# Kernel tuning notes

Measured on AMD Instinct MI355X. Metric: run time of the kernel, lower is better.

Reference implementation:

```python
import jax, jax.numpy as jnp
import numpy as np

B, N, L, H, D, IN = 512, 128, 10, 16, 8, 16
NT = B * N
E = NT * 16

def _lin(key, fan_in, shape):
    b = 1.0 / np.sqrt(fan_in)
    return jax.random.uniform(key, shape, jnp.float32, -b, b)

def setup_inputs() -> dict:
    key = jax.random.key(0)
    ks = jax.random.split(key, 12)
    x = jax.random.normal(ks[0], (NT, IN), jnp.float32)
    # within-graph random edges so to_dense_adj is well defined
    g = jax.random.randint(ks[1], (E,), 0, B)
    i = jax.random.randint(ks[2], (E,), 0, N)
    j = jax.random.randint(ks[3], (E,), 0, N)
    edge_index = jnp.stack([g * N + i, g * N + j]).astype(jnp.int32)
    return dict(
        x=x,
        gin_w1=_lin(ks[4], H, (2, L, H, H)),   # [ld/ud, layer, H, H]
        gin_b1=_lin(ks[5], H, (2, L, H)),
        gin_w2=_lin(ks[6], H, (2, L, H, H)),
        gin_b2=_lin(ks[7], H, (2, L, H)),
        mean_w=_lin(ks[8], H, (2, H, D)),
        mean_b=jnp.zeros((2, D), jnp.float32),
        std_w=_lin(ks[9], H, (2, H, D)),
        std_b=jnp.zeros((2, D), jnp.float32),
        edge_index=edge_index,
    )

def _encoder(x, w1, b1, w2, b2, mw, mb, sw, sb, src, dst):
    # PyG GIN stack: GINConv(MLP[Lin->ReLU->Lin]), eps=0, sum aggregation,
    # ReLU between layers (dropout = identity in eval mode).
    h = x
    for l in range(L):
        agg = jax.ops.segment_sum(h[src], dst, num_segments=NT)
        t = h + agg  # (1+eps)*x + sum_{j in N(i)} x_j with eps=0
        t = jnp.maximum(t @ w1[l] + b1[l], 0.0) @ w2[l] + b2[l]
        h = jnp.maximum(t, 0.0) if l < L - 1 else t
    mean = h @ mw + mb
    std = jax.nn.softplus(h @ sw + sb)
    return mean, std

def reference(x, gin_w1, gin_b1, gin_w2, gin_b2, mean_w, mean_b, std_w, std_b, edge_index):
    src, dst = edge_index[0], edge_index[1]
    enc = jax.vmap(_encoder, in_axes=(None, 0, 0, 0, 0, 0, 0, 0, 0, None, None))
    mean, std = enc(x, gin_w1, gin_b1, gin_w2, gin_b2,
                    mean_w, mean_b, std_w, std_b, src, dst)  # [2, NT, D]
    # reparameterized sample: eps ~ N(0,1) (prior.sample, detached)
    eps = jax.random.normal(jax.random.key(42), (2, NT, D), jnp.float32)
    z = mean + std * eps
    z_ld = z[0].reshape(B, N, D)
    z_ud = z[1].reshape(B, N, D)
    logits = jnp.einsum('bnd,bmd->bnm', z_ld, z_ud)  # per-graph inner-product decode
    dense_adj = jnp.zeros((B, N, N), jnp.float32).at[src // N, src % N, dst % N].add(1.0)
    n_pos = dense_adj.sum()
    posw = (B * N * N - n_pos) / n_pos
    # BCE-with-logits, pos_weight, reduction='sum'
    nll = jnp.sum(posw * dense_adj * jax.nn.softplus(-logits)
                  + (1.0 - dense_adj) * jax.nn.softplus(logits))
    # KL(N(mean,std) || N(0,1)), summed over both encoders
    kl = jnp.sum(-jnp.log(std) + 0.5 * (std * std + mean * mean) - 0.5)
    return nll, kl, jax.nn.sigmoid(logits), dense_adj
```

## Files before the change

kernel.cpp:

```cpp
#include <hip/hip_runtime.h>

#define B_    512
#define N_    128
#define L_    10
#define H_    16
#define D_    8
#define NT_   65536
#define E_    1048576
#define NNB_  8388608
#define CAP_  4096
#define CCAP_ 2816
#define HS_   20
#define PLANE_ (129*HS_ + 4)

__device__ __forceinline__ unsigned rotl32(unsigned v, int r){ return (v<<r)|(v>>(32-r)); }

__device__ __forceinline__ void threefry2x32(unsigned c0, unsigned c1, unsigned &o0, unsigned &o1){
  const unsigned ks0 = 0u, ks1 = 42u, ks2 = 0u ^ 42u ^ 0x1BD11BDAu;
  unsigned x0 = c0 + ks0, x1 = c1 + ks1;
#define TFR(r) { x0 += x1; x1 = rotl32(x1, r); x1 ^= x0; }
  TFR(13) TFR(15) TFR(26) TFR(6)   x0 += ks1; x1 += ks2 + 1u;
  TFR(17) TFR(29) TFR(16) TFR(24)  x0 += ks2; x1 += ks0 + 2u;
  TFR(13) TFR(15) TFR(26) TFR(6)   x0 += ks0; x1 += ks1 + 3u;
  TFR(17) TFR(29) TFR(16) TFR(24)  x0 += ks1; x1 += ks2 + 4u;
  TFR(13) TFR(15) TFR(26) TFR(6)   x0 += ks2; x1 += ks0 + 5u;
#undef TFR
  o0 = x0; o1 = x1;
}

__device__ __forceinline__ float erfinv_f(float x){
  float w = -log1pf(-x*x);
  float p;
  if (w < 5.0f) {
    w -= 2.5f;
    p = 2.81022636e-08f;
    p = fmaf(p, w, 3.43273939e-07f);
    p = fmaf(p, w, -3.5233877e-06f);
    p = fmaf(p, w, -4.39150654e-06f);
    p = fmaf(p, w, 0.00021858087f);
    p = fmaf(p, w, -0.00125372503f);
    p = fmaf(p, w, -0.00417768164f);
    p = fmaf(p, w, 0.246640727f);
    p = fmaf(p, w, 1.50140941f);
  } else {
    w = sqrtf(w) - 3.0f;
    p = -0.000200214257f;
    p = fmaf(p, w, 0.000100950558f);
    p = fmaf(p, w, 0.00134934322f);
    p = fmaf(p, w, -0.00367342844f);
    p = fmaf(p, w, 0.00573950773f);
    p = fmaf(p, w, -0.0076224613f);
    p = fmaf(p, w, 0.00943887047f);
    p = fmaf(p, w, 1.00167406f);
    p = fmaf(p, w, 2.83297682f);
  }
  return p * x;
}

__device__ __forceinline__ float softplus_f(float x){
  return fmaxf(x, 0.0f) + log1pf(expf(-fabsf(x)));
}

__device__ __forceinline__ void blockReduceAdd(double v, double* target){
  __shared__ double red[16];
  int lane = threadIdx.x & 63;
  int w    = threadIdx.x >> 6;
  #pragma unroll
  for(int off = 32; off > 0; off >>= 1) v += __shfl_down(v, off);
  if(lane == 0) red[w] = v;
  __syncthreads();
  if(threadIdx.x == 0){
    double s = red[0];
    int nw = (blockDim.x + 63) >> 6;
    for(int k = 1; k < nw; k++) s += red[k];
    atomicAdd(target, s);
  }
}

__global__ __launch_bounds__(256)
void k_bin(const int* __restrict__ ei, int* __restrict__ gcount,
           unsigned short* __restrict__ ebuf){
  __shared__ int cnt[512];
  __shared__ int gb[512];
  const int t = threadIdx.x;
  cnt[t] = 0; cnt[t + 256] = 0;
  __syncthreads();
  int kv[8];
  const int base = blockIdx.x * 2048;
  #pragma unroll
  for(int q = 0; q < 8; q++){
    int e = base + q*256 + t;
    int s = ei[e];
    int d = ei[E_ + e];
    int g = d >> 7;
    kv[q] = (g << 14) | ((s & 127) << 7) | (d & 127);
    atomicAdd(&cnt[g], 1);
  }
  __syncthreads();
  #pragma unroll
  for(int g = 0; g < 512; g += 256){
    int c = cnt[g + t];
    gb[g + t] = c ? atomicAdd(&gcount[g + t], c) : 0;
    cnt[g + t] = 0;
  }
  __syncthreads();
  #pragma unroll
  for(int q = 0; q < 8; q++){
    int g = kv[q] >> 14;
    int pos = atomicAdd(&cnt[g], 1);
    int idx = gb[g] + pos;
    if(idx < CAP_) ebuf[(size_t)g*CAP_ + idx] = (unsigned short)(kv[q] & 0x3FFF);
  }
}

__global__ __launch_bounds__(1024, 8)
void k_mega(const float* __restrict__ x, const unsigned short* __restrict__ ebuf,
            const int* __restrict__ gcount,
            const float* __restrict__ gw1, const float* __restrict__ gb1,
            const float* __restrict__ gw2, const float* __restrict__ gb2,
            const float* __restrict__ mw,  const float* __restrict__ mb,
            const float* __restrict__ sw,  const float* __restrict__ sb,
            float* __restrict__ z, double* acc){
  __shared__ __align__(16) float hh[2*PLANE_];
  __shared__ __align__(16) float agg_l[2*128*HS_];
  __shared__ __align__(16) float u_l[2*128*HS_];
  __shared__ __align__(16) unsigned short col_l[CCAP_];
  __shared__ int off_l[129];

  const int b = blockIdx.x, t = threadIdx.x;
  const int n  = t & 127;
  const int q  = __builtin_amdgcn_readfirstlane((t >> 7) & 3);
  const int e  = __builtin_amdgcn_readfirstlane(t >> 9);
  const int q4 = q * 4;

  int* cnt = (int*)hh;

  if(t < 128) cnt[t] = 0;
  {
    uint4 s128; s128.x = s128.y = s128.z = s128.w = 0x00800080u;
    uint4* c4 = (uint4*)col_l;
    if(t < CCAP_/8) c4[t] = s128;
  }
  __syncthreads();

  int ec = gcount[b]; if(ec > CAP_) ec = CAP_;
  const unsigned short* eb = ebuf + (size_t)b*CAP_;
  for(int i = t; i < ec; i += 1024) atomicAdd(&cnt[eb[i] & 127], 1);
  __syncthreads();

  if(t < 64){
    int lane = t;
    int a0 = (cnt[lane]      + 3) & ~3;
    int a1 = (cnt[64 + lane] + 3) & ~3;
    int s0 = a0, s1 = a1;
    #pragma unroll
    for(int o = 1; o < 64; o <<= 1){
      int v0 = __shfl_up(s0, o);
      int v1 = __shfl_up(s1, o);
      if(lane >= o){ s0 += v0; s1 += v1; }
    }
    int totA = __shfl(s0, 63);
    off_l[lane]      = s0 - a0;
    off_l[64 + lane] = totA + s1 - a1;
    if(lane == 63) off_l[128] = totA + s1;
    cnt[lane] = 0; cnt[64 + lane] = 0;
  }
  __syncthreads();

  for(int i = t; i < ec; i += 1024){
    int pk = eb[i];
    int d = pk & 127;
    int pos = atomicAdd(&cnt[d], 1);
    int idx = off_l[d] + pos;
    if(idx < CCAP_) col_l[idx] = (unsigned short)(pk >> 7);
  }
  __syncthreads();
  const int r0 = off_l[n], r1 = off_l[n + 1];

  if(t < 512){
    const float4* x4 = (const float4*)x + (size_t)b*512;
    float4 v = x4[t];
    int row = t >> 2, c = (t & 3)*4;
    *(float4*)&hh[row*HS_ + c]          = v;
    *(float4*)&hh[PLANE_ + row*HS_ + c] = v;
  }
  if(t < 16){ hh[128*HS_ + t] = 0.0f; hh[PLANE_ + 128*HS_ + t] = 0.0f; }
  __syncthreads();

  const float* hb   = hh    + e*PLANE_;
  float*       aggb = agg_l + e*(128*HS_);
  float*       ub   = u_l   + e*(128*HS_);
  const float* w1g = gw1 + e*(L_*256);
  const float* w2g = gw2 + e*(L_*256);
  const float* b1g = gb1 + e*(L_*16);
  const float* b2g = gb2 + e*(L_*16);

  for(int l = 0; l < L_; l++){
    float ag0, ag1, ag2, ag3;
    {
      float4 s = *(const float4*)&hb[n*HS_ + q4];
      ag0 = s.x; ag1 = s.y; ag2 = s.z; ag3 = s.w;
    }
    for(int r = r0; r < r1; r += 4){
      ushort4 c4 = *(const ushort4*)&col_l[r];
      float4 v0 = *(const float4*)&hb[c4.x*HS_ + q4];
      float4 v1 = *(const float4*)&hb[c4.y*HS_ + q4];
      float4 v2 = *(const float4*)&hb[c4.z*HS_ + q4];
      float4 v3 = *(const float4*)&hb[c4.w*HS_ + q4];
      ag0 += v0.x + v1.x + v2.x + v3.x;
      ag1 += v0.y + v1.y + v2.y + v3.y;
      ag2 += v0.z + v1.z + v2.z + v3.z;
      ag3 += v0.w + v1.w + v2.w + v3.w;
    }
    *(float4*)&aggb[n*HS_ + q4] = make_float4(ag0, ag1, ag2, ag3);
    __syncthreads();

    float av[16];
    {
      const float4* ap = (const float4*)&aggb[n*HS_];
      float4 a0 = ap[0], a1 = ap[1], a2 = ap[2], a3 = ap[3];
      av[0]=a0.x; av[1]=a0.y; av[2]=a0.z; av[3]=a0.w;
      av[4]=a1.x; av[5]=a1.y; av[6]=a1.z; av[7]=a1.w;
      av[8]=a2.x; av[9]=a2.y; av[10]=a2.z; av[11]=a2.w;
      av[12]=a3.x; av[13]=a3.y; av[14]=a3.z; av[15]=a3.w;
    }
    const float* w1c = w1g + l*256 + q4;
    float u0 = b1g[l*16 + q4 + 0];
    float u1 = b1g[l*16 + q4 + 1];
    float u2 = b1g[l*16 + q4 + 2];
    float u3 = b1g[l*16 + q4 + 3];
    #pragma unroll
    for(int k = 0; k < 16; k++){
      float a = av[k];
      const float* wr = w1c + k*16;
      u0 = fmaf(a, wr[0], u0);
      u1 = fmaf(a, wr[1], u1);
      u2 = fmaf(a, wr[2], u2);
      u3 = fmaf(a, wr[3], u3);
    }
    u0 = fmaxf(u0, 0.0f); u1 = fmaxf(u1, 0.0f);
    u2 = fmaxf(u2, 0.0f); u3 = fmaxf(u3, 0.0f);
    *(float4*)&ub[n*HS_ + q4] = make_float4(u0, u1, u2, u3);
    __syncthreads();

    float uv[16];
    {
      const float4* up = (const float4*)&ub[n*HS_];
      float4 a0 = up[0], a1 = up[1], a2 = up[2], a3 = up[3];
      uv[0]=a0.x; uv[1]=a0.y; uv[2]=a0.z; uv[3]=a0.w;
      uv[4]=a1.x; uv[5]=a1.y; uv[6]=a1.z; uv[7]=a1.w;
      uv[8]=a2.x; uv[9]=a2.y; uv[10]=a2.z; uv[11]=a2.w;
      uv[12]=a3.x; uv[13]=a3.y; uv[14]=a3.z; uv[15]=a3.w;
    }
    const float* w2c = w2g + l*256 + q4;
    float o0 = b2g[l*16 + q4 + 0];
    float o1 = b2g[l*16 + q4 + 1];
    float o2 = b2g[l*16 + q4 + 2];
    float o3 = b2g[l*16 + q4 + 3];
    #pragma unroll
    for(int k = 0; k < 16; k++){
      float a = uv[k];
      const float* wr = w2c + k*16;
      o0 = fmaf(a, wr[0], o0);
      o1 = fmaf(a, wr[1], o1);
      o2 = fmaf(a, wr[2], o2);
      o3 = fmaf(a, wr[3], o3);
    }
    if(l < L_ - 1){
      o0 = fmaxf(o0, 0.0f); o1 = fmaxf(o1, 0.0f);
      o2 = fmaxf(o2, 0.0f); o3 = fmaxf(o3, 0.0f);
    }
    *(float4*)&hh[e*PLANE_ + n*HS_ + q4] = make_float4(o0, o1, o2, o3);
    __syncthreads();
  }

  float hv[16];
  {
    const float4* hp = (const float4*)&hb[n*HS_];
    float4 a0 = hp[0], a1 = hp[1], a2 = hp[2], a3 = hp[3];
    hv[0]=a0.x; hv[1]=a0.y; hv[2]=a0.z; hv[3]=a0.w;
    hv[4]=a1.x; hv[5]=a1.y; hv[6]=a1.z; hv[7]=a1.w;
    hv[8]=a2.x; hv[9]=a2.y; hv[10]=a2.z; hv[11]=a2.w;
    hv[12]=a3.x; hv[13]=a3.y; hv[14]=a3.z; hv[15]=a3.w;
  }
  const float* mwg = mw + e*128; const float* mbg = mb + e*8;
  const float* swg = sw + e*128; const float* sbg = sb + e*8;
  double kll = 0.0;
  float zv[2];
  unsigned nodeBase = ((unsigned)e*NT_ + (unsigned)(b*128 + n))*8u;
  #pragma unroll
  for(int dd = 0; dd < 2; dd++){
    int d = q*2 + dd;
    float mm = mbg[d], ss = sbg[d];
    #pragma unroll
    for(int k = 0; k < 16; k++){
      mm = fmaf(hv[k], mwg[k*8 + d], mm);
      ss = fmaf(hv[k], swg[k*8 + d], ss);
    }
    float stdv = softplus_f(ss);
    unsigned o0, o1; threefry2x32(0u, nodeBase + (unsigned)d, o0, o1);
    unsigned bits = o0 ^ o1;
    float uu = __uint_as_float((bits >> 9) | 0x3f800000u) - 1.0f;
    const float lo = -0.99999994f;
    float uval = fmaxf(lo, fmaf(uu, 2.0f, lo));
    float eps = 1.41421356f * erfinv_f(uval);
    zv[dd] = mm + stdv * eps;
    float stdc = fmaxf(stdv, 1e-37f);
    float term = 0.5f*(stdv*stdv + mm*mm) - logf(stdc) - 0.5f;
    if(!(term == term) || term > 1e30f) term = 1e30f;
    kll += (double)term;
  }
  *(float2*)&z[nodeBase + (unsigned)(q*2)] = make_float2(zv[0], zv[1]);
  blockReduceAdd(kll, acc + 1);
}

#define TSB_ 132
__global__ __launch_bounds__(256, 8)
void k_decode(const float* __restrict__ z, const unsigned short* __restrict__ ebuf,
              const int* __restrict__ gcount, float* __restrict__ sig,
              float* __restrict__ adj, double* acc){
  __shared__ float zl[256];
  __shared__ float zu[1152];
  __shared__ unsigned tile32[32*TSB_/4];
  const int b = blockIdx.x, cy = blockIdx.y, t = threadIdx.x;
  const int row0 = cy * 32;
  const float* zld = z + (size_t)b*1024 + (size_t)row0*8;
  const float* zud = z + (size_t)NT_*8 + (size_t)b*1024;
  for(int k = t; k < 1024; k += 256) zu[(k >> 3)*9 + (k & 7)] = zud[k];
  zl[t] = zld[t];
  for(int k = t; k < 32*TSB_/4; k += 256) tile32[k] = 0u;
  __syncthreads();
  {
    int ec = gcount[b]; if(ec > CAP_) ec = CAP_;
    const unsigned short* eb = ebuf + (size_t)b*CAP_;
    for(int qq = t; qq < ec; qq += 256){
      int pk = eb[qq];
      int r = (pk >> 7) - row0;
      if((unsigned)r < 32u){
        int cell = r*TSB_ + (pk & 127);
        atomicAdd(&tile32[cell >> 2], 1u << ((cell & 3)*8));
      }
    }
  }
  __syncthreads();
  double local = 0.0;
  float* sigb = sig + (size_t)b*16384 + (size_t)row0*128;
  float* adjb = adj + (size_t)b*16384 + (size_t)row0*128;
  for(int it = 0; it < 4; it++){
    int base = it*1024 + t*4;
    int n = base >> 7, mcol = base & 127;
    const float* za = &zl[n*8];
    float xs[4];
    #pragma unroll
    for(int c = 0; c < 4; c++){
      const float* zb = &zu[(mcol + c)*9];
      float xx = 0.0f;
      #pragma unroll
      for(int d = 0; d < 8; d++) xx = fmaf(za[d], zb[d], xx);
      xs[c] = xx;
    }
    unsigned packed = tile32[(n*TSB_ + mcol) >> 2];
    float4 av;
    av.x = (float)( packed        & 0xFF);
    av.y = (float)((packed >> 8)  & 0xFF);
    av.z = (float)((packed >> 16) & 0xFF);
    av.w = (float)((packed >> 24) & 0xFF);
    float ads[4] = {av.x, av.y, av.z, av.w};
    float sgs[4];
    float fl = 0.0f;
    #pragma unroll
    for(int c = 0; c < 4; c++){
      float xx = xs[c];
      sgs[c] = 1.0f / (1.0f + expf(-xx));
      float cc  = log1pf(expf(-fabsf(xx)));
      float spp = fmaxf(xx, 0.0f) + cc;
      float spn = fmaxf(-xx, 0.0f) + cc;
      fl += 7.0f*ads[c]*spn + (1.0f - ads[c])*spp;
    }
    local += (double)fl;
    ((float4*)(sigb + base))[0] = make_float4(sgs[0], sgs[1], sgs[2], sgs[3]);
    ((float4*)(adjb + base))[0] = av;
  }
  blockReduceAdd(local, acc + 0);
}

__device__ __forceinline__ float clamp_finite(double v){
  if(v != v) return 0.0f;
  if(v >  3.3e38) return  3.3e38f;
  if(v < -3.3e38) return -3.3e38f;
  return (float)v;
}
__global__ void k_final(const double* __restrict__ acc, float* __restrict__ out){
  if(threadIdx.x == 0){
    out[0] = clamp_finite(acc[0]);
    out[1] = clamp_finite(acc[1]);
  }
}

extern "C" void kernel_launch(void* const* d_in, const int* in_sizes, int n_in,
                              void* d_out, int out_size, void* d_ws, size_t ws_size,
                              hipStream_t stream){
  const float* x   = (const float*)d_in[0];
  const float* gw1 = (const float*)d_in[1];
  const float* gb1 = (const float*)d_in[2];
  const float* gw2 = (const float*)d_in[3];
  const float* gb2 = (const float*)d_in[4];
  const float* mw  = (const float*)d_in[5];
  const float* mb  = (const float*)d_in[6];
  const float* sw  = (const float*)d_in[7];
  const float* sb  = (const float*)d_in[8];
  const int*   ei  = (const int*)d_in[9];

  float* out = (float*)d_out;
  float* sig = out + 2;
  float* adj = out + 2 + NNB_;

  char* ws = (char*)d_ws;
  int*            gcount = (int*)(ws);
  double*         acc    = (double*)(ws + 2048);
  unsigned short* ebuf   = (unsigned short*)(ws + 4096);
  float*          z      = (float*)(ws + 4096 + 2*512*CAP_);

  hipMemsetAsync(ws, 0, 4096, stream);

  k_bin   <<<E_/2048, 256, 0, stream>>>(ei, gcount, ebuf);
  k_mega  <<<B_, 1024, 0, stream>>>(x, ebuf, gcount, gw1, gb1, gw2, gb2,
                                    mw, mb, sw, sb, z, acc);
  k_decode<<<dim3(B_, 4), 256, 0, stream>>>(z, ebuf, gcount, sig, adj, acc);
  k_final <<<1, 64, 0, stream>>>(acc, out);
}
```

Measured before the change: 241.5 us.

## Sort edges in shared memory before scatter and restructure decode per column

```diff
diff --git a/kernel.cpp b/kernel.cpp
--- a/kernel.cpp
+++ b/kernel.cpp
@@ -77,39 +77,72 @@
   }
 }
 
-__global__ __launch_bounds__(256)
+__global__ __launch_bounds__(1024)
 void k_bin(const int* __restrict__ ei, int* __restrict__ gcount,
            unsigned short* __restrict__ ebuf){
+  __shared__ int skv[4096];
   __shared__ int cnt[512];
   __shared__ int gb[512];
+  __shared__ int off[512];
+  __shared__ int wtot[8];
   const int t = threadIdx.x;
-  cnt[t] = 0; cnt[t + 256] = 0;
-  __syncthreads();
-  int kv[8];
-  const int base = blockIdx.x * 2048;
-  #pragma unroll
-  for(int q = 0; q < 8; q++){
-    int e = base + q*256 + t;
+  if(t < 512) cnt[t] = 0;
+  __syncthreads();
+  int kv[4];
+  const int base = blockIdx.x * 4096;
+  #pragma unroll
+  for(int k = 0; k < 4; k++){
+    int e = base + k*1024 + t;
     int s = ei[e];
     int d = ei[E_ + e];
     int g = d >> 7;
-    kv[q] = (g << 14) | ((s & 127) << 7) | (d & 127);
+    kv[k] = (g << 14) | ((s & 127) << 7) | (d & 127);
     atomicAdd(&cnt[g], 1);
   }
   __syncthreads();
-  #pragma unroll
-  for(int g = 0; g < 512; g += 256){
-    int c = cnt[g + t];
-    gb[g + t] = c ? atomicAdd(&gcount[g + t], c) : 0;
-    cnt[g + t] = 0;
-  }
-  __syncthreads();
-  #pragma unroll
-  for(int q = 0; q < 8; q++){
-    int g = kv[q] >> 14;
+  int intra = 0;
+  if(t < 512){
+    int lane = t & 63;
+    int myc = cnt[t];
+    int s = myc;
+    #pragma unroll
+    for(int o = 1; o < 64; o <<= 1){
+      int v = __shfl_up(s, o);
+      if(lane >= o) s += v;
+    }
+    intra = s - myc;
+    if(lane == 63) wtot[t >> 6] = s;
+    gb[t] = myc ? atomicAdd(&gcount[t], myc) : 0;
+  }
+  __syncthreads();
+  if(t < 8){
+    int v = wtot[t];
+    int s = v;
+    #pragma unroll
+    for(int o = 1; o < 8; o <<= 1){
+      int u = __shfl_up(s, o);
+      if(t >= o) s += u;
+    }
+    wtot[t] = s - v;
+  }
+  if(t < 512) cnt[t] = 0;
+  __syncthreads();
+  if(t < 512) off[t] = intra + wtot[t >> 6];
+  __syncthreads();
+  #pragma unroll
+  for(int k = 0; k < 4; k++){
+    int g = kv[k] >> 14;
     int pos = atomicAdd(&cnt[g], 1);
-    int idx = gb[g] + pos;
-    if(idx < CAP_) ebuf[(size_t)g*CAP_ + idx] = (unsigned short)(kv[q] & 0x3FFF);
+    skv[off[g] + pos] = kv[k];
+  }
+  __syncthreads();
+  #pragma unroll
+  for(int k = 0; k < 4; k++){
+    int i = k*1024 + t;
+    int v = skv[i];
+    int g = v >> 14;
+    int idx = gb[g] + (i - off[g]);
+    if(idx < CAP_) ebuf[(size_t)g*CAP_ + idx] = (unsigned short)(v & 0x3FFF);
   }
 }
 
@@ -315,18 +348,19 @@
 }
 
 #define TSB_ 132
+#define ZUS_ 10
 __global__ __launch_bounds__(256, 8)
 void k_decode(const float* __restrict__ z, const unsigned short* __restrict__ ebuf,
               const int* __restrict__ gcount, float* __restrict__ sig,
               float* __restrict__ adj, double* acc){
   __shared__ float zl[256];
-  __shared__ float zu[1152];
+  __shared__ float zu[128*ZUS_];
   __shared__ unsigned tile32[32*TSB_/4];
   const int b = blockIdx.x, cy = blockIdx.y, t = threadIdx.x;
   const int row0 = cy * 32;
   const float* zld = z + (size_t)b*1024 + (size_t)row0*8;
   const float* zud = z + (size_t)NT_*8 + (size_t)b*1024;
-  for(int k = t; k < 1024; k += 256) zu[(k >> 3)*9 + (k & 7)] = zud[k];
+  for(int k = t; k < 1024; k += 256) zu[(k >> 3)*ZUS_ + (k & 7)] = zud[k];
   zl[t] = zld[t];
   for(int k = t; k < 32*TSB_/4; k += 256) tile32[k] = 0u;
   __syncthreads();
@@ -343,45 +377,33 @@
     }
   }
   __syncthreads();
-  double local = 0.0;
+  const int c  = t & 127;
+  const int rh = t >> 7;
+  float zb[8];
+  #pragma unroll
+  for(int d = 0; d < 8; d++) zb[d] = zu[c*ZUS_ + d];
   float* sigb = sig + (size_t)b*16384 + (size_t)row0*128;
   float* adjb = adj + (size_t)b*16384 + (size_t)row0*128;
-  for(int it = 0; it < 4; it++){
-    int base = it*1024 + t*4;
-    int n = base >> 7, mcol = base & 127;
-    const float* za = &zl[n*8];
-    float xs[4];
-    #pragma unroll
-    for(int c = 0; c < 4; c++){
-      const float* zb = &zu[(mcol + c)*9];
-      float xx = 0.0f;
-      #pragma unroll
-      for(int d = 0; d < 8; d++) xx = fmaf(za[d], zb[d], xx);
-      xs[c] = xx;
-    }
-    unsigned packed = tile32[(n*TSB_ + mcol) >> 2];
-    float4 av;
-    av.x = (float)( packed        & 0xFF);
-    av.y = (float)((packed >> 8)  & 0xFF);
-    av.z = (float)((packed >> 16) & 0xFF);
-    av.w = (float)((packed >> 24) & 0xFF);
-    float ads[4] = {av.x, av.y, av.z, av.w};
-    float sgs[4];
-    float fl = 0.0f;
-    #pragma unroll
-    for(int c = 0; c < 4; c++){
-      float xx = xs[c];
-      sgs[c] = 1.0f / (1.0f + expf(-xx));
-      float cc  = log1pf(expf(-fabsf(xx)));
-      float spp = fmaxf(xx, 0.0f) + cc;
-      float spn = fmaxf(-xx, 0.0f) + cc;
-      fl += 7.0f*ads[c]*spn + (1.0f - ads[c])*spp;
-    }
-    local += (double)fl;
-    ((float4*)(sigb + base))[0] = make_float4(sgs[0], sgs[1], sgs[2], sgs[3]);
-    ((float4*)(adjb + base))[0] = av;
-  }
-  blockReduceAdd(local, acc + 0);
+  const int sh = (c & 3)*8;
+  float fl = 0.0f;
+  #pragma unroll
+  for(int rs = 0; rs < 16; rs++){
+    int r = rh*16 + rs;
+    const float* za = &zl[r*8];
+    float xx = 0.0f;
+    #pragma unroll
+    for(int d = 0; d < 8; d++) xx = fmaf(za[d], zb[d], xx);
+    unsigned packed = tile32[(r*TSB_ + c) >> 2];
+    float ad = (float)((packed >> sh) & 0xFF);
+    float sg = 1.0f / (1.0f + expf(-xx));
+    float cc  = log1pf(expf(-fabsf(xx)));
+    float spp = fmaxf(xx, 0.0f) + cc;
+    float spn = fmaxf(-xx, 0.0f) + cc;
+    fl += 7.0f*ad*spn + (1.0f - ad)*spp;
+    sigb[r*128 + c] = sg;
+    adjb[r*128 + c] = ad;
+  }
+  blockReduceAdd((double)fl, acc + 0);
 }
 
 __device__ __forceinline__ float clamp_finite(double v){
@@ -423,7 +445,7 @@
 
   hipMemsetAsync(ws, 0, 4096, stream);
 
-  k_bin   <<<E_/2048, 256, 0, stream>>>(ei, gcount, ebuf);
+  k_bin   <<<E_/4096, 1024, 0, stream>>>(ei, gcount, ebuf);
   k_mega  <<<B_, 1024, 0, stream>>>(x, ebuf, gcount, gw1, gb1, gw2, gb2,
                                     mw, mb, sw, sb, z, acc);
   k_decode<<<dim3(B_, 4), 256, 0, stream>>>(z, ebuf, gcount, sig, adj, acc);
```

Result: faster. 219.4 us (-9.1%).
